# Kernel tuning notes

Hardware: AMD Instinct MI355X
Metric: run time of the kernel (lower is better)

The kernel has to match this reference:

```python
import jax, jax.numpy as jnp
import numpy as np
import math

B, S, D, H = 2, 2048, 1024, 16
DK = D // H
SCALE = math.sqrt(DK)
NEG_BIG = -1e9


def setup_inputs() -> dict:
    key = jax.random.key(0)
    ks = jax.random.split(key, 7)
    x = jax.random.normal(ks[0], (B, S, D), dtype=jnp.float32)
    # additive causal mask: 0 on/below diagonal, -inf above
    causal = jnp.triu(jnp.ones((S, S), dtype=bool), k=1)
    mask = jnp.where(causal, -jnp.inf, 0.0).astype(jnp.float32)
    key_padding_mask = jax.random.bernoulli(ks[1], 0.1, (B, S))
    init = 1.0 / math.sqrt(D)
    Wq = jax.random.normal(ks[2], (D, D), dtype=jnp.float32) * init
    Wk = jax.random.normal(ks[3], (D, D), dtype=jnp.float32) * init
    Wv = jax.random.normal(ks[4], (D, D), dtype=jnp.float32) * init
    Wo = jax.random.normal(ks[5], (D, D), dtype=jnp.float32) * init
    bo = jnp.zeros((D,), dtype=jnp.float32)
    return {"x": x, "mask": mask, "key_padding_mask": key_padding_mask,
            "Wq": Wq, "Wk": Wk, "Wv": Wv, "Wo": Wo, "bo": bo}


def reference(x, mask, key_padding_mask, Wq, Wk, Wv, Wo, bo):
    b, s, d = x.shape
    # project and split heads -> [B,H,S,Dk]
    def heads(W):
        return jnp.einsum('bsd,de->bse', x, W).reshape(b, s, H, DK).transpose(0, 2, 1, 3)
    Q, K, V = heads(Wq), heads(Wk), heads(Wv)
    scores = jnp.einsum('bhqd,bhkd->bhqk', Q, K) / SCALE          # [B,H,S,S]
    scores = scores + mask[None, None]                            # additive attn mask
    scores = jnp.where(key_padding_mask[:, None, None, :], -jnp.inf, scores)
    # rows whose max is -inf (fully masked) get all scores set to -1e9
    max_scores = jnp.max(scores, axis=-1, keepdims=True)
    scores = jnp.where(jnp.isinf(max_scores), NEG_BIG, scores)
    attn = jax.nn.softmax(scores, axis=-1)
    attn = jnp.where(jnp.isnan(attn), 0.0, attn)
    # dropout is identity in eval mode
    ctx = jnp.einsum('bhqk,bhkd->bhqd', attn, V)                  # [B,H,S,Dk]
    ctx = ctx.transpose(0, 2, 1, 3).reshape(b, s, d)
    return jnp.einsum('bsd,de->bse', ctx, Wo) + bo
```

## Files before the change

### kernel.cpp

```cpp
#include <hip/hip_runtime.h>
#include <stdint.h>

#define NB 2
#define NS 2048
#define ND 1024
#define NH 16
#define NDK 64

typedef __attribute__((ext_vector_type(8))) short s8v;
typedef __attribute__((ext_vector_type(4))) float f4v;
typedef __attribute__((ext_vector_type(4))) unsigned short us4v;
typedef __attribute__((ext_vector_type(8))) unsigned short us8v;
typedef __attribute__((ext_vector_type(2))) uint32_t u2v;

__device__ __forceinline__ unsigned short f2bf(float f) {
  uint32_t u = __builtin_bit_cast(uint32_t, f);
  u = (u + 0x7fffu + ((u >> 16) & 1u)) >> 16;
  return (unsigned short)u;
}
__device__ __forceinline__ float bf2f(unsigned short h) {
  uint32_t u = ((uint32_t)h) << 16;
  return __builtin_bit_cast(float, u);
}
__device__ __forceinline__ uint32_t cvtpk(float lo, float hi) {
  uint32_t r;
  asm("v_cvt_pk_bf16_f32 %0, %1, %2" : "=v"(r) : "v"(lo), "v"(hi));
  return r;
}

__device__ __forceinline__ void gload16(const void* g, void* l) {
  __builtin_amdgcn_global_load_lds(
      (const __attribute__((address_space(1))) void*)g,
      (__attribute__((address_space(3))) void*)l, 16, 0, 0);
}

__global__ void k_convert_x(const float* __restrict__ x, unsigned short* __restrict__ xbf) {
  int i = (blockIdx.x * 256 + threadIdx.x) * 4;
  float4 v = *(const float4*)(x + i);
  us4v o;
  o[0] = f2bf(v.x); o[1] = f2bf(v.y); o[2] = f2bf(v.z); o[3] = f2bf(v.w);
  *(us4v*)(xbf + i) = o;
}

__global__ void k_transpose_w(const float* __restrict__ Wq, const float* __restrict__ Wk,
                              const float* __restrict__ Wv, const float* __restrict__ Wo,
                              unsigned short* __restrict__ wt_qkv, unsigned short* __restrict__ wt_o) {
  __shared__ float tls[64][65];
  int bid = blockIdx.x;
  int mat = bid >> 8;
  int tile = bid & 255;
  int tk = tile >> 4, tn = tile & 15;
  const float* W = (mat == 0) ? Wq : (mat == 1) ? Wk : (mat == 2) ? Wv : Wo;
  int t = threadIdx.x;
  int lr = t >> 2;
  int lc0 = (t & 3) * 16;
  const float* src = W + (size_t)(tk * 64 + lr) * 1024 + tn * 64 + lc0;
#pragma unroll
  for (int j = 0; j < 16; j += 4) {
    float4 v = *(const float4*)(src + j);
    tls[lr][lc0 + j + 0] = v.x; tls[lr][lc0 + j + 1] = v.y;
    tls[lr][lc0 + j + 2] = v.z; tls[lr][lc0 + j + 3] = v.w;
  }
  __syncthreads();
  float scale = (mat == 0) ? 0.125f : 1.0f;
  int nr = t >> 2, kc0 = (t & 3) * 16;
  unsigned short* dst = ((mat < 3) ? (wt_qkv + (size_t)(mat * 1024 + tn * 64 + nr) * 1024)
                                   : (wt_o + (size_t)(tn * 64 + nr) * 1024)) + tk * 64 + kc0;
  us8v o0, o1;
#pragma unroll
  for (int j = 0; j < 8; j++) o0[j] = f2bf(tls[kc0 + j][nr] * scale);
#pragma unroll
  for (int j = 0; j < 8; j++) o1[j] = f2bf(tls[kc0 + 8 + j][nr] * scale);
  *(us8v*)(dst) = o0;
  *(us8v*)(dst + 8) = o1;
}

template <int MODE>
__global__ __launch_bounds__(256) void k_gemm(const unsigned short* __restrict__ A,
                                              const unsigned short* __restrict__ Bt,
                                              unsigned short* __restrict__ qklin,
                                              unsigned short* __restrict__ vt,
                                              const float* __restrict__ bias,
                                              float* __restrict__ out, int ntx) {
  __shared__ unsigned short lds_a[2][128 * 64];
  __shared__ unsigned short lds_b[2][128 * 64];
  const int K = 1024;
  int bid = blockIdx.x;
  int qc = gridDim.x >> 3;
  int swz = (bid & 7) * qc + (bid >> 3);
  int m0 = (swz / ntx) * 128, n0 = (swz % ntx) * 128;
  int tid = threadIdx.x, lane = tid & 63, w = tid >> 6;
  int wm = w >> 1, wn = w & 1;
  int g = lane >> 4, c0 = lane & 15;
  int rrel = lane >> 3;
  int gran = lane & 7;
  f4v acc[4][4];
#pragma unroll
  for (int mi = 0; mi < 4; mi++)
#pragma unroll
    for (int ni = 0; ni < 4; ni++) acc[mi][ni] = (f4v){0.f, 0.f, 0.f, 0.f};

#pragma unroll
  for (int i = 0; i < 4; i++) {
    int r = 32 * w + 8 * i + rrel;
    gload16(A + (size_t)(m0 + r) * K + 8 * (gran ^ rrel),
            (void*)(lds_a[0] + (32 * w + 8 * i) * 64));
    gload16(Bt + (size_t)(n0 + r) * K + 8 * (gran ^ rrel),
            (void*)(lds_b[0] + (32 * w + 8 * i) * 64));
  }
  __syncthreads();

  for (int kt = 0; kt < K / 64; ++kt) {
    int cur = kt & 1;
    if (kt < K / 64 - 1) {
#pragma unroll
      for (int i = 0; i < 4; i++) {
        int r = 32 * w + 8 * i + rrel;
        gload16(A + (size_t)(m0 + r) * K + (kt + 1) * 64 + 8 * (gran ^ rrel),
                (void*)(lds_a[cur ^ 1] + (32 * w + 8 * i) * 64));
        gload16(Bt + (size_t)(n0 + r) * K + (kt + 1) * 64 + 8 * (gran ^ rrel),
                (void*)(lds_b[cur ^ 1] + (32 * w + 8 * i) * 64));
      }
    }
#pragma unroll
    for (int c = 0; c < 2; c++) {
      s8v af[4], bfr[4];
#pragma unroll
      for (int mi = 0; mi < 4; mi++) {
        int row = 64 * wm + 16 * mi + c0;
        af[mi] = *(const s8v*)(lds_a[cur] + row * 64 + 8 * ((g + 4 * c) ^ (c0 & 7)));
      }
#pragma unroll
      for (int ni = 0; ni < 4; ni++) {
        int row = 64 * wn + 16 * ni + c0;
        bfr[ni] = *(const s8v*)(lds_b[cur] + row * 64 + 8 * ((g + 4 * c) ^ (c0 & 7)));
      }
#pragma unroll
      for (int mi = 0; mi < 4; mi++)
#pragma unroll
        for (int ni = 0; ni < 4; ni++)
          acc[mi][ni] = __builtin_amdgcn_mfma_f32_16x16x32_bf16(af[mi], bfr[ni], acc[mi][ni], 0, 0, 0);
    }
    __syncthreads();
  }

#pragma unroll
  for (int mi = 0; mi < 4; mi++)
#pragma unroll
    for (int ni = 0; ni < 4; ni++)
#pragma unroll
      for (int r = 0; r < 4; r++) {
        int m = m0 + 64 * wm + 16 * mi + 4 * g + r;
        int n = n0 + 64 * wn + 16 * ni + c0;
        float v = acc[mi][ni][r];
        if (MODE == 0) {
          unsigned short hv = f2bf(v);
          if (n < 2048) {
            qklin[(size_t)m * 2048 + n] = hv;
          } else {
            int b = m >> 11, s = m & 2047;
            int hh = (n - 2048) >> 6, dk = n & 63;
            vt[(size_t)((b * 16 + hh) * 64 + dk) * 2048 + s] = hv;
          }
        } else {
          out[(size_t)m * 1024 + n] = v + bias[n];
        }
      }
}

__global__ void k_vmean(const unsigned short* __restrict__ vt, float* __restrict__ vmean) {
  int row = blockIdx.x * 4 + (threadIdx.x >> 6);
  int lane = threadIdx.x & 63;
  const unsigned short* p = vt + (size_t)row * 2048 + lane * 32;
  float s = 0.f;
#pragma unroll
  for (int j = 0; j < 32; j += 8) {
    us8v v = *(const us8v*)(p + j);
#pragma unroll
    for (int e = 0; e < 8; e++) s += bf2f(v[e]);
  }
#pragma unroll
  for (int m = 1; m < 64; m <<= 1) s += __shfl_xor(s, m);
  if (lane == 0) vmean[row] = s * (1.0f / 2048.0f);
}

__global__ __launch_bounds__(256) void k_attn(const unsigned short* __restrict__ qklin,
                                              const unsigned short* __restrict__ vt,
                                              const int* __restrict__ kpm,
                                              const float* __restrict__ vmean,
                                              unsigned short* __restrict__ ctx) {
  __shared__ unsigned short lds_k[2][64 * 64];
  __shared__ unsigned short lds_v[64 * 64];
  __shared__ unsigned short p_lds[4][16 * 64];
  int wg = blockIdx.x;
  int qt = 31 - (wg >> 5), bh = wg & 31;
  int b = bh >> 4, h = bh & 15;
  int tid = threadIdx.x, lane = tid & 63, w = tid >> 6;
  int g = lane >> 4, c0 = lane & 15;
  int q0 = qt * 64 + w * 16;
  unsigned short* pl = p_lds[w];
  int rrel = lane >> 3, gran = lane & 7;

  const unsigned short* ksrc0 = qklin + (size_t)(b * NS) * 2048 + 1024 + h * 64;
  const unsigned short* vsrc0 = vt + (size_t)(bh * 64) * 2048;

  const unsigned short* qbase = qklin + (size_t)(b * NS + q0 + c0) * 2048 + h * 64 + 8 * g;
  s8v qf0 = *(const s8v*)(qbase);
  s8v qf1 = *(const s8v*)(qbase + 32);

  f4v cacc[4];
#pragma unroll
  for (int d = 0; d < 4; d++) cacc[d] = (f4v){0.f, 0.f, 0.f, 0.f};
  float m_s = -1e30f, l_s = 0.f;
  int qrow = q0 + c0;

#pragma unroll
  for (int i = 0; i < 2; i++) {
    int r = 16 * w + 8 * i + rrel;
    gload16(ksrc0 + (size_t)r * 2048 + 8 * (gran ^ rrel),
            (void*)(lds_k[0] + (16 * w + 8 * i) * 64));
  }
  __syncthreads();

  int nkt = qt + 1;
  for (int it = 0; it < nkt; ++it) {
    int kb = it * 64;
    int cur = it & 1;
#pragma unroll
    for (int i = 0; i < 2; i++) {
      int r = 16 * w + 8 * i + rrel;
      gload16(vsrc0 + (size_t)r * 2048 + kb + 8 * (gran ^ rrel),
              (void*)(lds_v + (16 * w + 8 * i) * 64));
    }
    if (it < qt) {
#pragma unroll
      for (int i = 0; i < 2; i++) {
        int r = 16 * w + 8 * i + rrel;
        gload16(ksrc0 + (size_t)(kb + 64 + r) * 2048 + 8 * (gran ^ rrel),
                (void*)(lds_k[cur ^ 1] + (16 * w + 8 * i) * 64));
      }
    }
    int kp = kpm[b * NS + kb + lane];
    uint64_t padmask = __ballot(kp != 0);
    f4v sacc[4];
#pragma unroll
    for (int t = 0; t < 4; t++) {
      int row = 16 * t + c0;
      s8v kf0 = *(const s8v*)(lds_k[cur] + row * 64 + 8 * (g ^ (c0 & 7)));
      s8v kf1 = *(const s8v*)(lds_k[cur] + row * 64 + 8 * ((4 + g) ^ (c0 & 7)));
      f4v z = (f4v){0.f, 0.f, 0.f, 0.f};
      z = __builtin_amdgcn_mfma_f32_16x16x32_bf16(kf0, qf0, z, 0, 0, 0);
      z = __builtin_amdgcn_mfma_f32_16x16x32_bf16(kf1, qf1, z, 0, 0, 0);
      sacc[t] = z;
    }
    int thr = qrow - kb;
    uint64_t cmask = (thr >= 63) ? ~0ull : ((2ull << thr) - 1ull);
    uint64_t valid = cmask & ~padmask;
    float p[4][4];
    float mx = -1e30f;
#pragma unroll
    for (int t = 0; t < 4; t++) {
      uint32_t nib = (uint32_t)(valid >> (16 * t + 4 * g)) & 0xFu;
#pragma unroll
      for (int r = 0; r < 4; r++) {
        float s = sacc[t][r];
        s = ((nib >> r) & 1u) ? s : -1e30f;
        p[t][r] = s;
      }
      mx = fmaxf(mx, fmaxf(fmaxf(p[t][0], p[t][1]), fmaxf(p[t][2], p[t][3])));
    }
    mx = fmaxf(mx, __shfl_xor(mx, 16));
    mx = fmaxf(mx, __shfl_xor(mx, 32));
    float mnew = fmaxf(m_s, mx);
    float a = __expf(m_s - mnew);
    float rs = 0.f;
#pragma unroll
    for (int t = 0; t < 4; t++)
#pragma unroll
      for (int r = 0; r < 4; r++) {
        float e = __expf(p[t][r] - mnew);
        p[t][r] = e;
        rs += e;
      }
    rs += __shfl_xor(rs, 16);
    rs += __shfl_xor(rs, 32);
    rs = (mnew > -1e29f) ? rs : 0.f;
    l_s = l_s * a + rs;
    m_s = mnew;
    {
      int ybase = 20 * g;
#pragma unroll
      for (int r = 0; r < 4; r++) {
        float ar = __shfl(a, ybase + r);
#pragma unroll
        for (int d = 0; d < 4; d++) cacc[d][r] *= ar;
      }
    }
#pragma unroll
    for (int t = 0; t < 4; t++) {
      u2v pk;
      pk[0] = cvtpk(p[t][0], p[t][1]);
      pk[1] = cvtpk(p[t][2], p[t][3]);
      int gr = (2 * t + (g >> 1)) ^ (c0 & 7);
      *(u2v*)((char*)pl + c0 * 128 + gr * 16 + 8 * (g & 1)) = pk;
    }
    __syncthreads();
#pragma unroll
    for (int c = 0; c < 2; c++) {
      int off = c0 * 128 + 16 * g + 64 * c;
      off ^= (c0 & 7) << 4;
      s8v pf = *(const s8v*)((const char*)pl + off);
#pragma unroll
      for (int d = 0; d < 4; d++) {
        int row = 16 * d + c0;
        s8v vf = *(const s8v*)(lds_v + row * 64 + 8 * ((4 * c + g) ^ (c0 & 7)));
        cacc[d] = __builtin_amdgcn_mfma_f32_16x16x32_bf16(pf, vf, cacc[d], 0, 0, 0);
      }
    }
    __syncthreads();
  }
  float lq[4];
  {
    int ybase = 20 * g;
#pragma unroll
    for (int r = 0; r < 4; r++) lq[r] = __shfl(l_s, ybase + r);
  }
#pragma unroll
  for (int d = 0; d < 4; d++)
#pragma unroll
    for (int r = 0; r < 4; r++) {
      int q = q0 + 4 * g + r;
      float l = lq[r];
      float v = (l > 0.f) ? cacc[d][r] / l : vmean[bh * 64 + 16 * d + c0];
      ctx[(size_t)(b * NS + q) * ND + h * 64 + 16 * d + c0] = f2bf(v);
    }
}

extern "C" void kernel_launch(void* const* d_in, const int* in_sizes, int n_in,
                              void* d_out, int out_size, void* d_ws, size_t ws_size,
                              hipStream_t stream) {
  const float* x  = (const float*)d_in[0];
  const int* kpm  = (const int*)d_in[2];
  const float* Wq = (const float*)d_in[3];
  const float* Wk = (const float*)d_in[4];
  const float* Wv = (const float*)d_in[5];
  const float* Wo = (const float*)d_in[6];
  const float* bo = (const float*)d_in[7];

  char* ws = (char*)d_ws;
  unsigned short* xbf   = (unsigned short*)(ws);
  unsigned short* wtqkv = (unsigned short*)(ws + 8u * 1024 * 1024);
  unsigned short* wto   = (unsigned short*)(ws + 14u * 1024 * 1024);
  unsigned short* vt    = (unsigned short*)(ws + 16u * 1024 * 1024);
  float* vmean          = (float*)(ws + 24u * 1024 * 1024);
  unsigned short* ctx   = xbf;
  unsigned short* qklin = (unsigned short*)d_out;

  k_convert_x<<<4096, 256, 0, stream>>>(x, xbf);
  k_transpose_w<<<1024, 256, 0, stream>>>(Wq, Wk, Wv, Wo, wtqkv, wto);
  k_gemm<0><<<768, 256, 0, stream>>>(xbf, wtqkv, qklin, vt, nullptr, nullptr, 24);
  k_vmean<<<512, 256, 0, stream>>>(vt, vmean);
  k_attn<<<1024, 256, 0, stream>>>(qklin, vt, kpm, vmean, ctx);
  k_gemm<1><<<256, 256, 0, stream>>>(ctx, wto, nullptr, nullptr, bo, (float*)d_out, 8);
}
```

Baseline: 144.5 us.

## Triple-buffer GEMM K-loop with explicit vmcnt waits and remap block tiles

The projection GEMM moves from a double-buffered to a triple-buffered LDS pipeline. It prefetches two K-tiles ahead and uses partial `s_waitcnt vmcnt` waits with raw barriers instead of a full `__syncthreads` per iteration, so global-load latency is hidden better. The block-to-tile mapping also changes to a fixed grouping of 4 M-tiles per XCD slot, aimed at L2 reuse. In exchange, LDS per block grows to 96KB, which may cut blocks per CU, and the mapping now assumes specific grid shapes.

New measurement: 152.1 us. 1.05x slower.

```diff
diff --git a/kernel.cpp b/kernel.cpp
--- a/kernel.cpp
+++ b/kernel.cpp
@@ -82,13 +82,14 @@
                                               unsigned short* __restrict__ vt,
                                               const float* __restrict__ bias,
                                               float* __restrict__ out, int ntx) {
-  __shared__ unsigned short lds_a[2][128 * 64];
-  __shared__ unsigned short lds_b[2][128 * 64];
+  __shared__ unsigned short lds_a[3][128 * 64];
+  __shared__ unsigned short lds_b[3][128 * 64];
   const int K = 1024;
+  const int NT = K / 64;
   int bid = blockIdx.x;
-  int qc = gridDim.x >> 3;
-  int swz = (bid & 7) * qc + (bid >> 3);
-  int m0 = (swz / ntx) * 128, n0 = (swz % ntx) * 128;
+  int x = bid & 7, local = bid >> 3;
+  int m0 = (x * 4 + (local & 3)) * 128;
+  int n0 = (local >> 2) * 128;
   int tid = threadIdx.x, lane = tid & 63, w = tid >> 6;
   int wm = w >> 1, wn = w & 1;
   int g = lane >> 4, c0 = lane & 15;
@@ -100,28 +101,27 @@
 #pragma unroll
     for (int ni = 0; ni < 4; ni++) acc[mi][ni] = (f4v){0.f, 0.f, 0.f, 0.f};
 
-#pragma unroll
-  for (int i = 0; i < 4; i++) {
-    int r = 32 * w + 8 * i + rrel;
-    gload16(A + (size_t)(m0 + r) * K + 8 * (gran ^ rrel),
-            (void*)(lds_a[0] + (32 * w + 8 * i) * 64));
-    gload16(Bt + (size_t)(n0 + r) * K + 8 * (gran ^ rrel),
-            (void*)(lds_b[0] + (32 * w + 8 * i) * 64));
-  }
-  __syncthreads();
-
-  for (int kt = 0; kt < K / 64; ++kt) {
-    int cur = kt & 1;
-    if (kt < K / 64 - 1) {
-#pragma unroll
-      for (int i = 0; i < 4; i++) {
-        int r = 32 * w + 8 * i + rrel;
-        gload16(A + (size_t)(m0 + r) * K + (kt + 1) * 64 + 8 * (gran ^ rrel),
-                (void*)(lds_a[cur ^ 1] + (32 * w + 8 * i) * 64));
-        gload16(Bt + (size_t)(n0 + r) * K + (kt + 1) * 64 + 8 * (gran ^ rrel),
-                (void*)(lds_b[cur ^ 1] + (32 * w + 8 * i) * 64));
-      }
-    }
+#define STAGE(kt_, buf_)                                                        \
+  do {                                                                          \
+    int koff = (kt_)*64;                                                        \
+    _Pragma("unroll") for (int i = 0; i < 4; i++) {                             \
+      int r = 32 * w + 8 * i + rrel;                                            \
+      gload16(A + (size_t)(m0 + r) * K + koff + 8 * (gran ^ rrel),              \
+              (void*)(lds_a[buf_] + (32 * w + 8 * i) * 64));                    \
+      gload16(Bt + (size_t)(n0 + r) * K + koff + 8 * (gran ^ rrel),             \
+              (void*)(lds_b[buf_] + (32 * w + 8 * i) * 64));                    \
+    }                                                                           \
+  } while (0)
+
+  STAGE(0, 0);
+  STAGE(1, 1);
+  asm volatile("s_waitcnt vmcnt(8)" ::: "memory");
+  __builtin_amdgcn_s_barrier();
+  __builtin_amdgcn_sched_barrier(0);
+
+  for (int kt = 0; kt < NT; ++kt) {
+    int cur = kt % 3;
+    if (kt + 2 < NT) STAGE(kt + 2, (kt + 2) % 3);
 #pragma unroll
     for (int c = 0; c < 2; c++) {
       s8v af[4], bfr[4];
@@ -141,8 +141,17 @@
         for (int ni = 0; ni < 4; ni++)
           acc[mi][ni] = __builtin_amdgcn_mfma_f32_16x16x32_bf16(af[mi], bfr[ni], acc[mi][ni], 0, 0, 0);
     }
-    __syncthreads();
-  }
+    if (kt + 1 < NT) {
+      if (kt + 2 < NT) {
+        asm volatile("s_waitcnt vmcnt(8)" ::: "memory");
+      } else {
+        asm volatile("s_waitcnt vmcnt(0)" ::: "memory");
+      }
+      __builtin_amdgcn_s_barrier();
+      __builtin_amdgcn_sched_barrier(0);
+    }
+  }
+#undef STAGE
 
 #pragma unroll
   for (int mi = 0; mi < 4; mi++)
```
